# Kernel optimization log

Hardware: AMD Instinct MI355X
Metric: run time of the kernel (lower is better)

Reference implementation:

```python
import jax, jax.numpy as jnp
import numpy as np

V, E, H = 100000, 50, 64   # vocab, embedding dim, GRU hidden
B, T = 1024, 200           # batch, max playlist length


def setup_inputs() -> dict:
    key = jax.random.key(0)
    ks = jax.random.split(key, 12)
    ids = jax.random.randint(ks[0], (B, T), 1, V)
    lengths = jax.random.randint(ks[1], (B,), T // 4, T + 1)
    pos = jnp.arange(T)[None, :]
    input_tracks = jnp.where(pos < lengths[:, None], ids, 0)  # 0 = pad (mask_zero)
    s = 0.05
    p = lambda k, shp: jax.random.normal(k, shp, dtype=jnp.float32) * s
    z = lambda shp: jnp.zeros(shp, jnp.float32)
    return {
        "input_tracks": input_tracks,
        "emb": p(ks[2], (V, E)),
        "Wx_f": p(ks[3], (E, 3 * H)), "Wh_f": p(ks[4], (H, 3 * H)),
        "bi_f": z(3 * H), "br_f": z(3 * H),
        "Wx_b": p(ks[5], (E, 3 * H)), "Wh_b": p(ks[6], (H, 3 * H)),
        "bi_b": z(3 * H), "br_b": z(3 * H),
        "Wk": p(ks[7], (2 * H, H)), "bk": z(H),
        "Wq": p(ks[8], (H, H)), "bq": z(H),
        "We": p(ks[9], (H, 1)), "be": z(1),
    }


def _gru(x, mask, Wx, Wh, bi, br):
    """Keras GRU (reset_after=True) with masking; masked steps carry state.
    x: [B,T,E] float, mask: [B,T] bool. Returns (outputs [B,T,H], final state [B,H])."""
    gx = jnp.einsum('bte,eh->bth', x, Wx) + bi  # precompute input projections [B,T,3H]

    def step(h, inp):
        gxt, mt = inp                     # [B,3H], [B]
        gh = h @ Wh + br                  # [B,3H] recurrent projections (with recurrent bias)
        xz, xr, xh = jnp.split(gxt, 3, axis=-1)
        hz, hr, hn = jnp.split(gh, 3, axis=-1)
        zg = jax.nn.sigmoid(xz + hz)
        rg = jax.nn.sigmoid(xr + hr)
        hh = jnp.tanh(xh + rg * hn)
        h_new = zg * h + (1.0 - zg) * hh
        h_new = jnp.where(mt[:, None], h_new, h)  # carry state through padding
        return h_new, h_new

    h0 = jnp.zeros((x.shape[0], Wh.shape[0]), x.dtype)
    hT, outs = jax.lax.scan(step, h0, (gx.transpose(1, 0, 2), mask.T))
    return outs.transpose(1, 0, 2), hT


def reference(input_tracks, emb, Wx_f, Wh_f, bi_f, br_f, Wx_b, Wh_b, bi_b, br_b,
              Wk, bk, Wq, bq, We, be):
    mask = input_tracks != 0                       # [B,T]
    x = emb[input_tracks]                          # [B,T,E]
    out_f, h_f = _gru(x, mask, Wx_f, Wh_f, bi_f, br_f)
    out_b_rev, _ = _gru(x[:, ::-1], mask[:, ::-1], Wx_b, Wh_b, bi_b, br_b)
    out_b = out_b_rev[:, ::-1]
    out = jnp.concatenate([out_f, out_b], axis=-1)  # [B,T,2H]
    keys = out @ Wk + bk                            # [B,T,H]
    query = (h_f @ Wq + bq)[:, None, :]             # [B,1,H]
    energy = jnp.tanh(keys + query) @ We + be       # [B,T,1]
    energy = energy + (1.0 - mask.astype(jnp.float32))[:, :, None] * (-1e9)
    weights = jax.nn.softmax(energy, axis=1)        # softmax over time
    context = jnp.sum(weights * out, axis=1)        # [B,2H]
    return context
```

## Files before the change

kernel.cpp:

```cpp
#include <hip/hip_runtime.h>
#include <hip/hip_bf16.h>

#define VV 100000
#define EE 50
#define HH 64
#define BB 1024
#define TT 200

typedef float v4f __attribute__((ext_vector_type(4)));
typedef float f32x4 __attribute__((ext_vector_type(4)));
typedef _Float16 f16x8 __attribute__((ext_vector_type(8)));
typedef _Float16 f16x2 __attribute__((ext_vector_type(2)));

__device__ __forceinline__ float fsig(float x) {
    return 1.f / (1.f + __expf(-x));
}
__device__ __forceinline__ float ftanh(float x) {
    float e = __expf(2.f * x);
    return 1.f - 2.f / (e + 1.f);
}

__global__ __launch_bounds__(256) void embw_kernel(
    const float* __restrict__ emb,
    const float* __restrict__ Wx_f, const float* __restrict__ bi_f, const float* __restrict__ br_f,
    const float* __restrict__ Wx_b, const float* __restrict__ bi_b, const float* __restrict__ br_b,
    float* __restrict__ embW_f, float* __restrict__ embW_b)
{
    const float* Wx = blockIdx.y ? Wx_b : Wx_f;
    const float* bi = blockIdx.y ? bi_b : bi_f;
    const float* br = blockIdx.y ? br_b : br_f;
    float* embW     = blockIdx.y ? embW_b : embW_f;
    __shared__ float wx_lds[EE * 192];
    __shared__ float emb_lds[32 * EE];
    const int tid = threadIdx.x;
    const int v0 = blockIdx.x * 32;
    for (int i = tid; i < EE * 192; i += 256) wx_lds[i] = Wx[i];
    for (int i = tid; i < 32 * EE; i += 256) emb_lds[i] = emb[(size_t)v0 * EE + i];
    __syncthreads();
    const int cg = tid & 63;
    const int rg = tid >> 6;
    float acc[8][3];
    #pragma unroll
    for (int i = 0; i < 8; i++) {
        acc[i][0] = bi[cg] + br[cg];
        acc[i][1] = bi[cg + 64] + br[cg + 64];
        acc[i][2] = bi[cg + 128];
    }
    for (int k = 0; k < EE; k++) {
        const float wx0 = wx_lds[k * 192 + cg];
        const float wx1 = wx_lds[k * 192 + cg + 64];
        const float wx2 = wx_lds[k * 192 + cg + 128];
        #pragma unroll
        for (int i = 0; i < 8; i++) {
            const float ev = emb_lds[(rg * 8 + i) * EE + k];
            acc[i][0] = fmaf(ev, wx0, acc[i][0]);
            acc[i][1] = fmaf(ev, wx1, acc[i][1]);
            acc[i][2] = fmaf(ev, wx2, acc[i][2]);
        }
    }
    #pragma unroll
    for (int i = 0; i < 8; i++) {
        const int vrow = v0 + rg * 8 + i;
        const size_t row = (size_t)vrow * 192;
        const bool pad = (vrow == 0);
        embW[row + cg]       = pad ? 38.f : acc[i][0];
        embW[row + cg + 64]  = pad ? 0.f  : acc[i][1];
        embW[row + cg + 128] = pad ? 0.f  : acc[i][2];
    }
}

__global__ __launch_bounds__(256, 1) void gru14_kernel(
    const int* __restrict__ ids,
    const float* __restrict__ eW_f, const float* __restrict__ eW_b,
    const float* __restrict__ Wh_f, const float* __restrict__ br_f,
    const float* __restrict__ Wh_b, const float* __restrict__ br_b,
    _Float16* __restrict__ outb,
    float* __restrict__ hf_out)
{
    const int tid  = threadIdx.x;
    const int w    = tid >> 6;
    const int lane = tid & 63;
    const int l15  = lane & 15;
    const int lhi  = lane >> 4;
    const int dir  = blockIdx.y;
    const int b0   = blockIdx.x * 16;
    const float* eW = dir ? eW_b : eW_f;
    const float* Wh = dir ? Wh_b : Wh_f;
    const float* br = dir ? br_b : br_f;
    const int c  = 16 * w + l15;
    const int r0 = 4 * lhi;

    f16x8 bw[3][2];
    #pragma unroll
    for (int g = 0; g < 3; g++) {
        #pragma unroll
        for (int kt = 0; kt < 2; kt++) {
            #pragma unroll
            for (int jj = 0; jj < 8; jj++)
                bw[g][kt][jj] = (_Float16)Wh[(size_t)(32 * kt + 8 * lhi + jj) * 192 + 64 * g + c];
        }
    }
    const float brn = br[128 + c];

    __shared__ __align__(16) _Float16 hlds[2][16][88];
    __shared__ int idsT[TT * 16];
    for (int i = tid; i < TT * 16; i += 256)
        idsT[i] = ids[(size_t)(b0 + (i & 15)) * TT + (i >> 4)];
    for (int i = tid; i < 2 * 16 * 88; i += 256) ((_Float16*)hlds)[i] = (_Float16)0.f;
    float hold[4] = {0.f, 0.f, 0.f, 0.f};
    __syncthreads();

    const int t0 = dir ? (TT - 1) : 0;
    const int dt = dir ? -1 : 1;

    float gxA[3][4], gxB[3][4], gxC[3][4], gxD[3][4];

#define PREF(BANK, SF) { \
    const int tf_ = t0 + (SF) * dt; \
    _Pragma("unroll") \
    for (int r = 0; r < 4; r++) { \
        const int idq_ = idsT[tf_ * 16 + r0 + r]; \
        const float* p_ = eW + (size_t)idq_ * 192 + c; \
        BANK[0][r] = p_[0]; BANK[1][r] = p_[64]; BANK[2][r] = p_[128]; \
    } }

#define STEP(BANK, SCUR) { \
    const int t_ = t0 + (SCUR) * dt; \
    const int nxt_ = cur ^ 1; \
    const f16x8 a0_ = *(const f16x8*)&hlds[cur][l15][8 * lhi]; \
    const f16x8 a1_ = *(const f16x8*)&hlds[cur][l15][32 + 8 * lhi]; \
    f32x4 az0 = {0.f,0.f,0.f,0.f}, ar0 = {0.f,0.f,0.f,0.f}, an0 = {0.f,0.f,0.f,0.f}; \
    f32x4 az1 = {0.f,0.f,0.f,0.f}, ar1 = {0.f,0.f,0.f,0.f}, an1 = {0.f,0.f,0.f,0.f}; \
    az0 = __builtin_amdgcn_mfma_f32_16x16x32_f16(a0_, bw[0][0], az0, 0, 0, 0); \
    ar0 = __builtin_amdgcn_mfma_f32_16x16x32_f16(a0_, bw[1][0], ar0, 0, 0, 0); \
    an0 = __builtin_amdgcn_mfma_f32_16x16x32_f16(a0_, bw[2][0], an0, 0, 0, 0); \
    az1 = __builtin_amdgcn_mfma_f32_16x16x32_f16(a1_, bw[0][1], az1, 0, 0, 0); \
    ar1 = __builtin_amdgcn_mfma_f32_16x16x32_f16(a1_, bw[1][1], ar1, 0, 0, 0); \
    an1 = __builtin_amdgcn_mfma_f32_16x16x32_f16(a1_, bw[2][1], an1, 0, 0, 0); \
    _Pragma("unroll") \
    for (int r = 0; r < 4; r++) { \
        const float z_  = fsig(BANK[0][r] + (az0[r] + az1[r])); \
        const float rg_ = fsig(BANK[1][r] + (ar0[r] + ar1[r])); \
        const float hh_ = ftanh(BANK[2][r] + rg_ * (an0[r] + an1[r] + brn)); \
        const float hn_ = hh_ + z_ * (hold[r] - hh_); \
        hold[r] = hn_; \
        hlds[nxt_][r0 + r][c] = (_Float16)hn_; \
        outb[((size_t)(b0 + r0 + r) * TT + t_) * 128 + dir * 64 + c] = (_Float16)hn_; \
    } \
    cur = nxt_; \
    if ((SCUR) + 4 < TT) PREF(BANK, (SCUR) + 4) \
    asm volatile("s_waitcnt lgkmcnt(0)\n\ts_barrier" ::: "memory"); \
    __builtin_amdgcn_sched_barrier(0); }

    PREF(gxA, 0)
    PREF(gxB, 1)
    PREF(gxC, 2)
    PREF(gxD, 3)
    int cur = 0;
    for (int s = 0; s < TT; s += 4) {
        STEP(gxA, s)
        STEP(gxB, s + 1)
        STEP(gxC, s + 2)
        STEP(gxD, s + 3)
    }
#undef PREF
#undef STEP
    if (dir == 0) {
        #pragma unroll
        for (int r = 0; r < 4; r++)
            hf_out[(size_t)(b0 + r0 + r) * 64 + c] = hold[r];
    }
}

#define NTILE 13

__global__ __launch_bounds__(256) void attn9_kernel(
    const int* __restrict__ ids,
    const _Float16* __restrict__ outb,
    const float* __restrict__ hf,
    const float* __restrict__ Wk, const float* __restrict__ bk,
    const float* __restrict__ Wq, const float* __restrict__ bq,
    const float* __restrict__ We, const float* __restrict__ be,
    float* __restrict__ ctx)
{
    __shared__ __align__(16) _Float16 wk_sw[1024 * 8];
    __shared__ float q_lds[64];
    __shared__ float we_lds[64];
    __shared__ float e_lds[TT];
    __shared__ float part[4][128];
    const int b = blockIdx.x;
    const int tid = threadIdx.x;
    const int w = tid >> 6;
    const int lane = tid & 63;
    const int l15 = lane & 15;
    const int lhi = lane >> 4;

    #pragma unroll
    for (int i = 0; i < 4; i++) {
        const int slot = tid + 256 * i;
        const int s_l15 = slot & 15;
        const int s_nt  = (slot >> 4) & 3;
        const int s_lhi = (slot >> 6) & 3;
        const int s_ks  = slot >> 8;
        const int kbase = 32 * s_ks + 8 * s_lhi;
        const int col   = 16 * s_nt + s_l15;
        f16x8 v;
        #pragma unroll
        for (int jj = 0; jj < 8; jj++) v[jj] = (_Float16)Wk[(size_t)(kbase + jj) * 64 + col];
        *(f16x8*)&wk_sw[slot * 8] = v;
    }
    if (tid < 64) {
        float qc = bq[tid];
        const float* hfb = hf + (size_t)b * 64;
        for (int k = 0; k < 64; k++) qc = fmaf(hfb[k], Wq[k * 64 + tid], qc);
        q_lds[tid] = qc;
        we_lds[tid] = We[tid];
    }
    __syncthreads();

    for (int tile = w; tile < NTILE; tile += 4) {
        const int t0 = tile * 16;
        const int t = t0 + l15;
        f32x4 acc[4];
        #pragma unroll
        for (int nt = 0; nt < 4; nt++) { acc[nt][0] = 0.f; acc[nt][1] = 0.f; acc[nt][2] = 0.f; acc[nt][3] = 0.f; }
        #pragma unroll
        for (int ks = 0; ks < 4; ks++) {
            f16x8 a;
            if (t < TT) {
                a = *(const f16x8*)(outb + ((size_t)b * TT + t) * 128 + 32 * ks + 8 * lhi);
            } else {
                #pragma unroll
                for (int jj = 0; jj < 8; jj++) a[jj] = (_Float16)0.f;
            }
            #pragma unroll
            for (int nt = 0; nt < 4; nt++) {
                const f16x8 bf = *(const f16x8*)&wk_sw[(ks * 256 + lhi * 64 + nt * 16 + l15) * 8];
                acc[nt] = __builtin_amdgcn_mfma_f32_16x16x32_f16(a, bf, acc[nt], 0, 0, 0);
            }
        }
        float ep0 = 0.f, ep1 = 0.f, ep2 = 0.f, ep3 = 0.f;
        #pragma unroll
        for (int nt = 0; nt < 4; nt++) {
            const int c = 16 * nt + l15;
            const float qn = q_lds[c];
            const float wen = we_lds[c];
            ep0 = fmaf(wen, ftanh(acc[nt][0] + qn), ep0);
            ep1 = fmaf(wen, ftanh(acc[nt][1] + qn), ep1);
            ep2 = fmaf(wen, ftanh(acc[nt][2] + qn), ep2);
            ep3 = fmaf(wen, ftanh(acc[nt][3] + qn), ep3);
        }
        #pragma unroll
        for (int off = 1; off < 16; off <<= 1) {
            ep0 += __shfl_xor(ep0, off);
            ep1 += __shfl_xor(ep1, off);
            ep2 += __shfl_xor(ep2, off);
            ep3 += __shfl_xor(ep3, off);
        }
        if (l15 == 0) {
            const int rbase = t0 + 4 * lhi;
            if (rbase + 0 < TT) e_lds[rbase + 0] = ep0;
            if (rbase + 1 < TT) e_lds[rbase + 1] = ep1;
            if (rbase + 2 < TT) e_lds[rbase + 2] = ep2;
            if (rbase + 3 < TT) e_lds[rbase + 3] = ep3;
        }
    }
    __syncthreads();
    if (w == 0) {
        const float bev = be[0];
        for (int t = lane; t < TT; t += 64) {
            float e = e_lds[t] + bev;
            if (ids[(size_t)b * TT + t] == 0) e -= 1e9f;
            e_lds[t] = e;
        }
        float m = -1e30f;
        for (int t = lane; t < TT; t += 64) m = fmaxf(m, e_lds[t]);
        #pragma unroll
        for (int off = 32; off > 0; off >>= 1) m = fmaxf(m, __shfl_xor(m, off));
        float ssum = 0.f;
        for (int t = lane; t < TT; t += 64) { const float v = __expf(e_lds[t] - m); e_lds[t] = v; ssum += v; }
        #pragma unroll
        for (int off = 32; off > 0; off >>= 1) ssum += __shfl_xor(ssum, off);
        const float inv = 1.f / ssum;
        for (int t = lane; t < TT; t += 64) e_lds[t] *= inv;
    }
    __syncthreads();
    float c0 = 0.f, c1 = 0.f;
    for (int t = w; t < TT; t += 4) {
        const f16x2 hv = *(const f16x2*)(outb + ((size_t)b * TT + t) * 128 + 2 * lane);
        const float wt = e_lds[t];
        c0 = fmaf(wt, (float)hv[0], c0);
        c1 = fmaf(wt, (float)hv[1], c1);
    }
    part[w][2 * lane]     = c0;
    part[w][2 * lane + 1] = c1;
    __syncthreads();
    if (tid < 128)
        ctx[(size_t)b * 128 + tid] = part[0][tid] + part[1][tid] + part[2][tid] + part[3][tid];
}

template<bool USE_EMBW>
__global__ __launch_bounds__(192, 2) void gru_kernel(
    const int* __restrict__ ids,
    const float* __restrict__ embW_f, const float* __restrict__ embW_b,
    const float* __restrict__ emb,
    const float* __restrict__ Wx_f, const float* __restrict__ bi_f,
    const float* __restrict__ Wx_b, const float* __restrict__ bi_b,
    const float* __restrict__ Wh_f, const float* __restrict__ br_f,
    const float* __restrict__ Wh_b, const float* __restrict__ br_b,
    float* __restrict__ outb, float* __restrict__ hf_out)
{
    constexpr int R = 4;
    __shared__ float h_lds[R][64];
    __shared__ float rg_lds[R][64];
    __shared__ float hh_lds[R][64];
    __shared__ int ids_lds[R * TT];
    const int tid = threadIdx.x;
    const int w = tid >> 6;
    const int j = tid & 63;
    const int dir = blockIdx.y;
    const int b0 = blockIdx.x * R;
    const float* Wh   = dir ? Wh_b : Wh_f;
    const float* br   = dir ? br_b : br_f;
    const float* Wx   = dir ? Wx_b : Wx_f;
    const float* bi   = dir ? bi_b : bi_f;
    const int c = w * 64 + j;

    float whc[64];
    #pragma unroll
    for (int k = 0; k < 64; k++) whc[k] = Wh[k * 192 + c];
    const float brc = br[c];
    float wxc[EE];
    float bic = 0.f;
    if (!USE_EMBW) {
        #pragma unroll
        for (int k = 0; k < EE; k++) wxc[k] = Wx[k * 192 + c];
        bic = bi[c];
    }
    for (int i = tid; i < R * TT; i += 192) ids_lds[i] = ids[(size_t)b0 * TT + i];
    if (w == 0) {
        #pragma unroll
        for (int r = 0; r < R; r++) h_lds[r][j] = 0.f;
    }
    __syncthreads();

    for (int s = 0; s < TT; s++) {
        const int t = dir ? (TT - 1 - s) : s;
        int idv[R];
        float gxv[R], accv[R];
        #pragma unroll
        for (int r = 0; r < R; r++) idv[r] = ids_lds[r * TT + t];
        #pragma unroll
        for (int r = 0; r < R; r++) {
            float acc = bic;
            const float* er = emb + (size_t)idv[r] * EE;
            #pragma unroll
            for (int k = 0; k < EE; k++) acc = fmaf(er[k], wxc[k], acc);
            gxv[r] = acc;
        }
        #pragma unroll
        for (int r = 0; r < R; r++) {
            float acc = brc;
            const float4* h4 = (const float4*)(&h_lds[r][0]);
            #pragma unroll
            for (int k4 = 0; k4 < 16; k4++) {
                const float4 hv = h4[k4];
                acc = fmaf(hv.x, whc[4 * k4 + 0], acc);
                acc = fmaf(hv.y, whc[4 * k4 + 1], acc);
                acc = fmaf(hv.z, whc[4 * k4 + 2], acc);
                acc = fmaf(hv.w, whc[4 * k4 + 3], acc);
            }
            accv[r] = acc;
        }
        float zg[R] = {};
        if (w == 1) {
            #pragma unroll
            for (int r = 0; r < R; r++) rg_lds[r][j] = fsig(gxv[r] + accv[r]);
        } else if (w == 0) {
            #pragma unroll
            for (int r = 0; r < R; r++) zg[r] = fsig(gxv[r] + accv[r]);
        }
        __syncthreads();
        if (w == 2) {
            #pragma unroll
            for (int r = 0; r < R; r++)
                hh_lds[r][j] = ftanh(gxv[r] + rg_lds[r][j] * accv[r]);
        }
        __syncthreads();
        if (w == 0) {
            #pragma unroll
            for (int r = 0; r < R; r++) {
                const float hold = h_lds[r][j];
                float hnew = hold;
                if (idv[r] != 0) {
                    const float hh = hh_lds[r][j];
                    hnew = zg[r] * hold + (1.f - zg[r]) * hh;
                }
                h_lds[r][j] = hnew;
                outb[((size_t)(b0 + r) * TT + t) * 128 + dir * 64 + j] = hnew;
            }
        }
        __syncthreads();
    }
    if (dir == 0 && w == 0) {
        #pragma unroll
        for (int r = 0; r < R; r++) hf_out[(size_t)(b0 + r) * 64 + j] = h_lds[r][j];
    }
}

__global__ __launch_bounds__(256, 3) void attn_fp32_kernel(
    const int* __restrict__ ids,
    const float* __restrict__ outb, const float* __restrict__ hf,
    const float* __restrict__ Wk, const float* __restrict__ bk,
    const float* __restrict__ Wq, const float* __restrict__ bq,
    const float* __restrict__ We, const float* __restrict__ be,
    float* __restrict__ ctx)
{
    __shared__ float epart[2][TT];
    __shared__ float e_lds[TT];
    __shared__ float part[4][128];
    const int b = blockIdx.x;
    const int tid = threadIdx.x;
    const int w = tid >> 6;
    const int lane = tid & 63;
    const int cg = w & 1;
    const int tg = w >> 1;
    const int c = cg * 32 + (lane & 31);
    const int h = lane >> 5;
    float wkc[64];
    #pragma unroll
    for (int kk = 0; kk < 64; kk++) wkc[kk] = Wk[(size_t)(64 * h + kk) * 64 + c];
    float qc = bq[c] + bk[c];
    {
        const float4* hf4 = (const float4*)(hf + (size_t)b * 64);
        #pragma unroll
        for (int k4 = 0; k4 < 16; k4++) {
            const float4 hv = hf4[k4];
            qc = fmaf(hv.x, Wq[(4 * k4 + 0) * 64 + c], qc);
            qc = fmaf(hv.y, Wq[(4 * k4 + 1) * 64 + c], qc);
            qc = fmaf(hv.z, Wq[(4 * k4 + 2) * 64 + c], qc);
            qc = fmaf(hv.w, Wq[(4 * k4 + 3) * 64 + c], qc);
        }
    }
    const float wec = We[c];
    const float bev = be[0];
    for (int t = tg; t < TT; t += 2) {
        const float4* o4 = (const float4*)(outb + ((size_t)b * TT + t) * 128 + 64 * h);
        float a0 = 0.f, a1 = 0.f;
        #pragma unroll
        for (int i4 = 0; i4 < 16; i4++) {
            const float4 ov = o4[i4];
            a0 = fmaf(ov.x, wkc[4 * i4 + 0], a0);
            a1 = fmaf(ov.y, wkc[4 * i4 + 1], a1);
            a0 = fmaf(ov.z, wkc[4 * i4 + 2], a0);
            a1 = fmaf(ov.w, wkc[4 * i4 + 3], a1);
        }
        float key = a0 + a1;
        key += __shfl_xor(key, 32);
        float v = ftanh(key + qc) * wec;
        #pragma unroll
        for (int off = 16; off > 0; off >>= 1) v += __shfl_xor(v, off);
        if (lane == 0) epart[cg][t] = v;
    }
    __syncthreads();
    if (w == 0) {
        for (int t = lane; t < TT; t += 64) {
            float e = epart[0][t] + epart[1][t] + bev;
            if (ids[(size_t)b * TT + t] == 0) e -= 1e9f;
            e_lds[t] = e;
        }
        float m = -1e30f;
        for (int t = lane; t < TT; t += 64) m = fmaxf(m, e_lds[t]);
        #pragma unroll
        for (int off = 32; off > 0; off >>= 1) m = fmaxf(m, __shfl_xor(m, off));
        float ssum = 0.f;
        for (int t = lane; t < TT; t += 64) { const float v = __expf(e_lds[t] - m); e_lds[t] = v; ssum += v; }
        #pragma unroll
        for (int off = 32; off > 0; off >>= 1) ssum += __shfl_xor(ssum, off);
        const float inv = 1.f / ssum;
        for (int t = lane; t < TT; t += 64) e_lds[t] *= inv;
    }
    __syncthreads();
    float c0 = 0.f, c1 = 0.f;
    for (int t = w; t < TT; t += 4) {
        const float* orow = outb + ((size_t)b * TT + t) * 128;
        const float wt = e_lds[t];
        c0 = fmaf(wt, orow[lane], c0);
        c1 = fmaf(wt, orow[64 + lane], c1);
    }
    part[w][lane] = c0;
    part[w][64 + lane] = c1;
    __syncthreads();
    if (tid < 128)
        ctx[(size_t)b * 128 + tid] = part[0][tid] + part[1][tid] + part[2][tid] + part[3][tid];
}

extern "C" void kernel_launch(void* const* d_in, const int* in_sizes, int n_in,
                              void* d_out, int out_size, void* d_ws, size_t ws_size,
                              hipStream_t stream) {
    const int*   ids  = (const int*)d_in[0];
    const float* emb  = (const float*)d_in[1];
    const float* Wx_f = (const float*)d_in[2];
    const float* Wh_f = (const float*)d_in[3];
    const float* bi_f = (const float*)d_in[4];
    const float* br_f = (const float*)d_in[5];
    const float* Wx_b = (const float*)d_in[6];
    const float* Wh_b = (const float*)d_in[7];
    const float* bi_b = (const float*)d_in[8];
    const float* br_b = (const float*)d_in[9];
    const float* Wk   = (const float*)d_in[10];
    const float* bk   = (const float*)d_in[11];
    const float* Wq   = (const float*)d_in[12];
    const float* bq   = (const float*)d_in[13];
    const float* We   = (const float*)d_in[14];
    const float* be   = (const float*)d_in[15];
    float* ctx = (float*)d_out;

    const size_t embw_elems = (size_t)VV * 192;
    const size_t out_elems  = (size_t)BB * TT * 128;
    const size_t hf_elems   = (size_t)BB * 64;
    const size_t need = embw_elems * 2 * sizeof(float)
                      + out_elems * sizeof(_Float16)
                      + hf_elems * sizeof(float);

    if (ws_size >= need) {
        float* embW_f    = (float*)d_ws;
        float* embW_b    = embW_f + embw_elems;
        _Float16* outb16 = (_Float16*)(embW_b + embw_elems);
        float* hf = (float*)(outb16 + out_elems);
        embw_kernel<<<dim3(VV / 32, 2), 256, 0, stream>>>(
            emb, Wx_f, bi_f, br_f, Wx_b, bi_b, br_b, embW_f, embW_b);
        gru14_kernel<<<dim3(BB / 16, 2), 256, 0, stream>>>(
            ids, embW_f, embW_b, Wh_f, br_f, Wh_b, br_b, outb16, hf);
        attn9_kernel<<<BB, 256, 0, stream>>>(ids, outb16, hf, Wk, bk, Wq, bq, We, be, ctx);
    } else {
        float* outb = (float*)d_ws;
        float* hf   = outb + out_elems;
        gru_kernel<false><<<dim3(BB / 4, 2), 192, 0, stream>>>(
            ids, nullptr, nullptr, emb, Wx_f, bi_f, Wx_b, bi_b,
            Wh_f, br_f, Wh_b, br_b, outb, hf);
        attn_fp32_kernel<<<BB, 256, 0, stream>>>(ids, outb, hf, Wk, bk, Wq, bq, We, be, ctx);
    }
}
```

Baseline: 286.6 us.

## Split GRU across more blocks with four batch rows per block

The GRU kernel now handles 4 batch rows per block instead of 16, launching 512 blocks rather than 128 so more CUs run the serial recurrence. Input projections are fetched once per row and broadcast across lanes with shuffles. The 16-row MFMA tile is kept, so 12 of its rows are padding and wasted work, and only a quarter of the lanes write the hidden state. The aim is to shorten the latency-bound 200-step chain per block by using many more CUs in parallel.

```diff
diff --git a/kernel.cpp b/kernel.cpp
--- a/kernel.cpp
+++ b/kernel.cpp
@@ -69,7 +69,7 @@
     }
 }
 
-__global__ __launch_bounds__(256, 1) void gru14_kernel(
+__global__ __launch_bounds__(256, 1) void gru17_kernel(
     const int* __restrict__ ids,
     const float* __restrict__ eW_f, const float* __restrict__ eW_b,
     const float* __restrict__ Wh_f, const float* __restrict__ br_f,
@@ -83,12 +83,11 @@
     const int l15  = lane & 15;
     const int lhi  = lane >> 4;
     const int dir  = blockIdx.y;
-    const int b0   = blockIdx.x * 16;
+    const int b0   = blockIdx.x * 4;
     const float* eW = dir ? eW_b : eW_f;
     const float* Wh = dir ? Wh_b : Wh_f;
     const float* br = dir ? br_b : br_f;
-    const int c  = 16 * w + l15;
-    const int r0 = 4 * lhi;
+    const int c = 16 * w + l15;
 
     f16x8 bw[3][2];
     #pragma unroll
@@ -103,9 +102,9 @@
     const float brn = br[128 + c];
 
     __shared__ __align__(16) _Float16 hlds[2][16][88];
-    __shared__ int idsT[TT * 16];
-    for (int i = tid; i < TT * 16; i += 256)
-        idsT[i] = ids[(size_t)(b0 + (i & 15)) * TT + (i >> 4)];
+    __shared__ int idsT[TT * 4];
+    for (int i = tid; i < TT * 4; i += 256)
+        idsT[i] = ids[(size_t)(b0 + (i & 3)) * TT + (i >> 2)];
     for (int i = tid; i < 2 * 16 * 88; i += 256) ((_Float16*)hlds)[i] = (_Float16)0.f;
     float hold[4] = {0.f, 0.f, 0.f, 0.f};
     __syncthreads();
@@ -113,20 +112,25 @@
     const int t0 = dir ? (TT - 1) : 0;
     const int dt = dir ? -1 : 1;
 
-    float gxA[3][4], gxB[3][4], gxC[3][4], gxD[3][4];
+    float gxA[3], gxB[3], gxC[3], gxD[3];
 
 #define PREF(BANK, SF) { \
     const int tf_ = t0 + (SF) * dt; \
-    _Pragma("unroll") \
-    for (int r = 0; r < 4; r++) { \
-        const int idq_ = idsT[tf_ * 16 + r0 + r]; \
-        const float* p_ = eW + (size_t)idq_ * 192 + c; \
-        BANK[0][r] = p_[0]; BANK[1][r] = p_[64]; BANK[2][r] = p_[128]; \
-    } }
+    const int idq_ = idsT[tf_ * 4 + lhi]; \
+    const float* p_ = eW + (size_t)idq_ * 192 + c; \
+    BANK[0] = p_[0]; BANK[1] = p_[64]; BANK[2] = p_[128]; }
 
 #define STEP(BANK, SCUR) { \
     const int t_ = t0 + (SCUR) * dt; \
     const int nxt_ = cur ^ 1; \
+     \
+    float gz_[4], gr_[4], gn_[4]; \
+    _Pragma("unroll") \
+    for (int r = 0; r < 4; r++) { \
+        gz_[r] = __shfl(BANK[0], 16 * r + l15); \
+        gr_[r] = __shfl(BANK[1], 16 * r + l15); \
+        gn_[r] = __shfl(BANK[2], 16 * r + l15); \
+    } \
     const f16x8 a0_ = *(const f16x8*)&hlds[cur][l15][8 * lhi]; \
     const f16x8 a1_ = *(const f16x8*)&hlds[cur][l15][32 + 8 * lhi]; \
     f32x4 az0 = {0.f,0.f,0.f,0.f}, ar0 = {0.f,0.f,0.f,0.f}, an0 = {0.f,0.f,0.f,0.f}; \
@@ -139,13 +143,18 @@
     an1 = __builtin_amdgcn_mfma_f32_16x16x32_f16(a1_, bw[2][1], an1, 0, 0, 0); \
     _Pragma("unroll") \
     for (int r = 0; r < 4; r++) { \
-        const float z_  = fsig(BANK[0][r] + (az0[r] + az1[r])); \
-        const float rg_ = fsig(BANK[1][r] + (ar0[r] + ar1[r])); \
-        const float hh_ = ftanh(BANK[2][r] + rg_ * (an0[r] + an1[r] + brn)); \
+        const float z_  = fsig(gz_[r] + (az0[r] + az1[r])); \
+        const float rg2_ = fsig(gr_[r] + (ar0[r] + ar1[r])); \
+        const float hh_ = ftanh(gn_[r] + rg2_ * (an0[r] + an1[r] + brn)); \
         const float hn_ = hh_ + z_ * (hold[r] - hh_); \
         hold[r] = hn_; \
-        hlds[nxt_][r0 + r][c] = (_Float16)hn_; \
-        outb[((size_t)(b0 + r0 + r) * TT + t_) * 128 + dir * 64 + c] = (_Float16)hn_; \
+    } \
+    if (lhi == 0) { \
+        _Pragma("unroll") \
+        for (int r = 0; r < 4; r++) { \
+            hlds[nxt_][r][c] = (_Float16)hold[r]; \
+            outb[((size_t)(b0 + r) * TT + t_) * 128 + dir * 64 + c] = (_Float16)hold[r]; \
+        } \
     } \
     cur = nxt_; \
     if ((SCUR) + 4 < TT) PREF(BANK, (SCUR) + 4) \
@@ -165,10 +174,10 @@
     }
 #undef PREF
 #undef STEP
-    if (dir == 0) {
+    if (dir == 0 && lhi == 0) {
         #pragma unroll
         for (int r = 0; r < 4; r++)
-            hf_out[(size_t)(b0 + r0 + r) * 64 + c] = hold[r];
+            hf_out[(size_t)(b0 + r) * 64 + c] = hold[r];
     }
 }
 
@@ -530,7 +539,7 @@
         float* hf = (float*)(outb16 + out_elems);
         embw_kernel<<<dim3(VV / 32, 2), 256, 0, stream>>>(
             emb, Wx_f, bi_f, br_f, Wx_b, bi_b, br_b, embW_f, embW_b);
-        gru14_kernel<<<dim3(BB / 16, 2), 256, 0, stream>>>(
+        gru17_kernel<<<dim3(BB / 4, 2), 256, 0, stream>>>(
             ids, embW_f, embW_b, Wh_f, br_f, Wh_b, br_b, outb16, hf);
         attn9_kernel<<<BB, 256, 0, stream>>>(ids, outb16, hf, Wk, bk, Wq, bq, We, be, ctx);
     } else {
```

Result: slower. 374.2 us (+30.6%).
